# Optimization experiments

Hardware: AMD Instinct MI355X
Metric: run time of the kernel (lower is better)

## Reference

```python
import jax, jax.numpy as jnp
import numpy as np
import math

B, P, N, DM, H, DK, DH, DF = 2, 12, 170, 64, 8, 8, 32, 256
SQ = math.sqrt(DK)

def _ln(x, g, b):
    m = jnp.mean(x, -1, keepdims=True)
    v = jnp.var(x, -1, keepdims=True)
    return (x - m) / jnp.sqrt(v + 1e-5) * g + b

def _nozero_softmax(s):
    # faithful to nozero_softmax: mask = (s != 0), max over full row, +1e-5 in denom
    mask = (s != 0).astype(s.dtype)
    e = jnp.exp(s - jnp.max(s, -1, keepdims=True)) * mask
    return e / (jnp.sum(e, -1, keepdims=True) + 1e-5)

def _meta(c, w1, b1, w2, b2):
    # MetaLearner: [B,P,N,DM] -> [3,B,P,N,H,DK,DM]
    h = jax.nn.relu(c @ w1 + b1) @ w2 + b2
    h = h.reshape(c.shape[:3] + (3, H, DK, DM))
    return jnp.moveaxis(h, 3, 0)

def _mhlin(W, x):
    # multihead_linear_transform: per-position meta weight applied to x
    return jnp.einsum('bpnhkd,bpnd->bpnhk', W, x)

def _gdc(data, W1, W2):
    # Gated_Dynamic_Connection (noGC=False). data: [G,B,P,N,C]
    d = jnp.moveaxis(data, 0, 3)  # [B,P,N,G,C]
    a = jnp.einsum('bpngc,gcd->bpngd', d, W1)
    s = jax.nn.softmax(jax.nn.relu(jnp.einsum('bpngc,gcd->bpngd', d, W2)), axis=3)
    return jnp.sum(a * s, axis=3)  # [B,P,N,DM]

def _swish_gate(x, out, wg, bg, wo, bo):
    h = (x @ wg + bg) * out
    return (h * jax.nn.sigmoid(h)) @ wo + bo

def _spatial(Q, K, V, T):
    # adjacency-masked spatial attention. Dense-masked form is exactly the
    # scatter-into-zeros buffer of the original: zero where T==0, QK/sqrt(dk) on edges.
    s = jnp.einsum('bpihk,bpjhk->bphij', Q, K) / SQ
    Tb = T if T.ndim == 2 else T[:, :, None]  # adaptive graph [B,P,1,N,N]
    s = s * (Tb != 0)
    alpha = _nozero_softmax(s) * Tb
    return jnp.einsum('bphij,bpjhk->hbpik', alpha, V)  # [H,B,P,N,DK]

def _temporal(Q, K, V):
    s = jnp.einsum('bqnhk,bpnhk->bnhqp', Q, K) / SQ
    alpha = jax.nn.softmax(s, -1)
    return jnp.einsum('bnhqp,bpnhk->hbqnk', alpha, V)  # [H,B,P,N,DK]

def _retnet(Q, K, V, D):
    # multihead_temporal_regnet with g=1 leading dim folded in
    r = jnp.einsum('bqnhk,bpnhk->bnhqp', Q, K) / SQ
    r = r * D  # D: [H,P,P] causal decay
    rs = jnp.maximum(jnp.abs(jnp.sum(r, -1, keepdims=True)), 1.0)
    r = r / rs
    return jnp.einsum('bnhqp,bpnhk->hbqnk', r, V)  # [H,B,P,N,DK]

def _forward(x, c_x, enc, T, A, D, mr_w1, mr_b1, mr_w2, mr_b2, ms0_w1, ms0_b1, ms0_w2, ms0_b2, ms1_w1, ms1_b1, ms1_w2, ms1_b2, gr_W1, gr_W2, gs0_W1, gs0_W2, gs1_W1, gs1_W2, g2_W1, g2_W2, ge_W1, ge_W2, swr_wg, swr_bg, swr_wo, swr_bo, sws_wg, sws_bg, sws_wo, sws_bo, swe_wg, swe_bg, swe_wo, swe_bo, lnr_g, lnr_b, lns_g, lns_b, lne_g, lne_b, lnf_g, lnf_b, wq, wk, wv, f_w1, f_b1, f_w2, f_b2):
    # 1) RetNet-style temporal self retention (meta-learned QKV)
    W = _meta(c_x, mr_w1, mr_b1, mr_w2, mr_b2)
    o = _gdc(_retnet(_mhlin(W[0], x), _mhlin(W[1], x), _mhlin(W[2], x), D), gr_W1, gr_W2)
    o = _swish_gate(x, o, swr_wg, swr_bg, swr_wo, swr_bo)
    x1 = _ln(o + x, lnr_g, lnr_b)
    # 2) Spatial self attention: predefined graph + adaptive graph branches
    W0 = _meta(c_x, ms0_w1, ms0_b1, ms0_w2, ms0_b2)
    o0 = _gdc(_spatial(_mhlin(W0[0], x1), _mhlin(W0[1], x1), _mhlin(W0[2], x1), T), gs0_W1, gs0_W2)
    W1m = _meta(c_x, ms1_w1, ms1_b1, ms1_w2, ms1_b2)
    o1 = _gdc(_spatial(_mhlin(W1m[0], x1), _mhlin(W1m[1], x1), _mhlin(W1m[2], x1), A), gs1_W1, gs1_W2)
    o = _gdc(jnp.stack([o0, o1], 0), g2_W1, g2_W2)
    o = _swish_gate(x1, o, sws_wg, sws_bg, sws_wo, sws_bo)
    x2 = _ln(o + x1, lns_g, lns_b)
    # 3) Temporal encoder-decoder attention
    q = (x2 @ wq).reshape(B, P, N, H, DK)
    k = (enc @ wk).reshape(B, P, N, H, DK)
    v = (enc @ wv).reshape(B, P, N, H, DK)
    o = _gdc(_temporal(q, k, v), ge_W1, ge_W2)
    o = _swish_gate(x2, o, swe_wg, swe_bg, swe_wo, swe_bo)
    x3 = _ln(o + x2, lne_g, lne_b)
    # 4) FFN
    o = jax.nn.relu(x3 @ f_w1 + f_b1) @ f_w2 + f_b2
    return _ln(o + x3, lnf_g, lnf_b)


def setup_inputs() -> dict:
    key = jax.random.key(0)
    ks = iter(jax.random.split(key, 100))
    def rn(shape, s=0.05):
        return (jax.random.normal(next(ks), shape) * s).astype(jnp.float32)
    inp = {}
    inp['x'] = jax.random.normal(next(ks), (B, P, N, DM), jnp.float32)
    inp['c_x'] = jax.random.normal(next(ks), (B, P, N, DM), jnp.float32)
    inp['enc'] = jax.random.normal(next(ks), (B, P, N, DM), jnp.float32)
    mT = jax.random.uniform(next(ks), (N, N)) < 0.1
    inp['T'] = (jax.random.uniform(next(ks), (N, N)) * mT).astype(jnp.float32)
    mA = jax.random.uniform(next(ks), (B, P, N, N)) < 0.05
    inp['A'] = (jax.random.uniform(next(ks), (B, P, N, N)) * mA).astype(jnp.float32)
    q = np.arange(P)
    gam = 1.0 - 2.0 ** (-5.0 - np.arange(H))
    Dm = np.where(q[:, None] >= q[None, :], gam[:, None, None] ** (q[:, None] - q[None, :]), 0.0)
    inp['D'] = jnp.asarray(Dm, jnp.float32)  # [H,P,P]
    for p in ['mr', 'ms0', 'ms1']:
        inp[p + '_w1'] = rn((DM, DH)); inp[p + '_b1'] = jnp.zeros((DH,), jnp.float32)
        inp[p + '_w2'] = rn((DH, 3 * H * DK * DM)); inp[p + '_b2'] = jnp.zeros((3 * H * DK * DM,), jnp.float32)
    for p in ['gr', 'gs0', 'gs1', 'ge']:
        inp[p + '_W1'] = rn((H, DK, DM)); inp[p + '_W2'] = rn((H, DK, DM))
    inp['g2_W1'] = rn((2, DM, DM)); inp['g2_W2'] = rn((2, DM, DM))
    for p in ['swr', 'sws', 'swe']:
        inp[p + '_wg'] = rn((DM, DM)); inp[p + '_bg'] = jnp.zeros((DM,), jnp.float32)
        inp[p + '_wo'] = rn((DM, DM)); inp[p + '_bo'] = jnp.zeros((DM,), jnp.float32)
    for p in ['lnr', 'lns', 'lne', 'lnf']:
        inp[p + '_g'] = jnp.ones((DM,), jnp.float32); inp[p + '_b'] = jnp.zeros((DM,), jnp.float32)
    inp['wq'] = rn((DM, DM)); inp['wk'] = rn((DM, DM)); inp['wv'] = rn((DM, DM))
    inp['f_w1'] = rn((DM, DF)); inp['f_b1'] = jnp.zeros((DF,), jnp.float32)
    inp['f_w2'] = rn((DF, DM)); inp['f_b2'] = jnp.zeros((DM,), jnp.float32)
    return inp


def reference(x, c_x, enc, T, A, D, mr_w1, mr_b1, mr_w2, mr_b2, ms0_w1, ms0_b1, ms0_w2, ms0_b2, ms1_w1, ms1_b1, ms1_w2, ms1_b2, gr_W1, gr_W2, gs0_W1, gs0_W2, gs1_W1, gs1_W2, g2_W1, g2_W2, ge_W1, ge_W2, swr_wg, swr_bg, swr_wo, swr_bo, sws_wg, sws_bg, sws_wo, sws_bo, swe_wg, swe_bg, swe_wo, swe_bo, lnr_g, lnr_b, lns_g, lns_b, lne_g, lne_b, lnf_g, lnf_b, wq, wk, wv, f_w1, f_b1, f_w2, f_b2):
    return _forward(x, c_x, enc, T, A, D, mr_w1, mr_b1, mr_w2, mr_b2, ms0_w1, ms0_b1, ms0_w2, ms0_b2, ms1_w1, ms1_b1, ms1_w2, ms1_b2, gr_W1, gr_W2, gs0_W1, gs0_W2, gs1_W1, gs1_W2, g2_W1, g2_W2, ge_W1, ge_W2, swr_wg, swr_bg, swr_wo, swr_bo, sws_wg, sws_bg, sws_wo, sws_bo, swe_wg, swe_bg, swe_wo, swe_bo, lnr_g, lnr_b, lns_g, lns_b, lne_g, lne_b, lnf_g, lnf_b, wq, wk, wv, f_w1, f_b1, f_w2, f_b2)
```

## Files before the change

kernel.cpp:

```cpp
#include <hip/hip_runtime.h>
#include <hip/hip_bf16.h>
#include <math.h>

namespace {

constexpr int B_ = 2, P_ = 12, N_ = 170, DM_ = 64, H_ = 8, DK_ = 8, DH_ = 32, DF_ = 256;
constexpr int T_ = B_ * P_ * N_;
constexpr float SQRT_DK = 2.8284271247461903f;

constexpr int NG_ = 12;
constexpr int NC_ = 66;
constexpr int WFRAG_G = NG_ * NC_ * 64 * 8;

typedef __attribute__((ext_vector_type(4))) short short4v;
typedef __attribute__((ext_vector_type(8))) short short8v;
typedef __attribute__((ext_vector_type(4))) float float4v;

__device__ __forceinline__ unsigned short f2bf(float x) {
    union { float f; unsigned int u; } c; c.f = x;
    unsigned int r = (c.u + 0x7FFFu + ((c.u >> 16) & 1u)) >> 16;
    return (unsigned short)r;
}

__global__ void k_hr3(const float* __restrict__ c_x,
                      const float* __restrict__ w1a, const float* __restrict__ b1a,
                      const float* __restrict__ w1b, const float* __restrict__ b1b,
                      const float* __restrict__ w1c, const float* __restrict__ b1c,
                      float* __restrict__ hra, float* __restrict__ hrb,
                      float* __restrict__ hrc) {
    int z = blockIdx.y;
    const float* w1 = z == 0 ? w1a : (z == 1 ? w1b : w1c);
    const float* b1 = z == 0 ? b1a : (z == 1 ? b1b : b1c);
    float* hr = z == 0 ? hra : (z == 1 ? hrb : hrc);
    int idx = blockIdx.x * 256 + threadIdx.x;
    if (idx >= T_ * DH_) return;
    int t = idx / DH_, j = idx % DH_;
    float acc = b1[j];
    const float* cx = c_x + t * DM_;
    #pragma unroll
    for (int d = 0; d < DM_; ++d) acc += cx[d] * w1[d * DH_ + j];
    hr[idx] = fmaxf(acc, 0.f);
}

__global__ void k_wconv(const float* __restrict__ w2a, const float* __restrict__ b2a,
                        const float* __restrict__ w2b, const float* __restrict__ b2b,
                        const float* __restrict__ w2c, const float* __restrict__ b2c,
                        unsigned short* __restrict__ Wfrag) {
    int idx = blockIdx.x * 256 + threadIdx.x;
    if (idx >= 3 * NG_ * NC_ * 64) return;
    int lane = idx & 63;
    int c = (idx >> 6) % NC_;
    int ng = (idx >> 6) / NC_ % NG_;
    int g = idx / (64 * NC_ * NG_);
    const float* w2 = g == 0 ? w2a : (g == 1 ? w2b : w2c);
    const float* b2 = g == 0 ? b2a : (g == 1 ? b2b : b2c);
    int m = ng * 16 + (lane & 15);
    int u = c >> 1;
    int d0 = (c & 1) * 32 + (lane >> 4) * 8;
    const float* src = (u < DH_) ? (w2 + u * 12288 + m * 64 + d0) : (b2 + m * 64 + d0);
    short8v o;
    #pragma unroll
    for (int j = 0; j < 8; ++j) o[j] = (short)f2bf(src[j]);
    *(short8v*)(Wfrag + (size_t)idx * 8) = o;
}

__global__ __launch_bounds__(256) void k_meta_gemm2(
    const float* __restrict__ hr0, const float* __restrict__ hr1,
    const float* __restrict__ xin,
    const unsigned short* __restrict__ Wf0, const unsigned short* __restrict__ Wf1,
    float* __restrict__ out0, float* __restrict__ out1) {
    const int bz = blockIdx.z;
    const float* hr = bz ? hr1 : hr0;
    const unsigned short* Wf = bz ? Wf1 : Wf0;
    float* out = bz ? out1 : out0;

    const int tid = threadIdx.x;
    const int wv = tid >> 6, lane = tid & 63;
    const int l15 = lane & 15, quad = lane >> 4;
    const int g16 = blockIdx.x * 4 + wv;
    if (g16 >= 255) return;
    const int t = g16 * 16 + l15;
    const int nb = blockIdx.y;

    const float* xp = xin + t * 64 + quad * 8;
    float4v xa = *(const float4v*)(xp);
    float4v xb = *(const float4v*)(xp + 4);
    float4v xc = *(const float4v*)(xp + 32);
    float4v xd = *(const float4v*)(xp + 36);
    float xr[16] = {xa.x, xa.y, xa.z, xa.w, xb.x, xb.y, xb.z, xb.w,
                    xc.x, xc.y, xc.z, xc.w, xd.x, xd.y, xd.z, xd.w};

    const float* hrp = hr + t * 32;
    float4v acc[4] = {{0.f,0.f,0.f,0.f},{0.f,0.f,0.f,0.f},
                      {0.f,0.f,0.f,0.f},{0.f,0.f,0.f,0.f}};

    const unsigned short* wb = Wf + ((size_t)(nb * 4) * NC_ * 64 + lane) * 8;
    const size_t qstride = (size_t)NC_ * 64 * 8;
    const size_t cstride = 64 * 8;

    for (int u = 0; u < 33; ++u) {
        float hrv = (u < DH_) ? hrp[u] : 1.0f;
        short8v a0, a1;
        #pragma unroll
        for (int j = 0; j < 8; ++j) {
            a0[j] = (short)f2bf(hrv * xr[j]);
            a1[j] = (short)f2bf(hrv * xr[8 + j]);
        }
        const unsigned short* wc = wb + (size_t)(2 * u) * cstride;
        #pragma unroll
        for (int q = 0; q < 4; ++q) {
            short8v b0 = *(const short8v*)(wc + q * qstride);
            short8v b1 = *(const short8v*)(wc + q * qstride + cstride);
            acc[q] = __builtin_amdgcn_mfma_f32_16x16x32_bf16(a0, b0, acc[q], 0, 0, 0);
            acc[q] = __builtin_amdgcn_mfma_f32_16x16x32_bf16(a1, b1, acc[q], 0, 0, 0);
        }
    }

    #pragma unroll
    for (int q = 0; q < 4; ++q) {
        #pragma unroll
        for (int r = 0; r < 4; ++r) {
            int tt = g16 * 16 + quad * 4 + r;
            out[tt * 192 + nb * 64 + q * 16 + l15] = acc[q][r];
        }
    }
}

__global__ __launch_bounds__(256) void k_retnet(const float* __restrict__ qkv,
                                                const float* __restrict__ Dm,
                                                float* __restrict__ att) {
    const int bn = blockIdx.x;
    const int b = bn / N_, n = bn % N_;
    __shared__ float S[12][192];
    __shared__ float Ds[8 * 145];
    const int tid = threadIdx.x;
    for (int e = tid; e < 12 * 192; e += 256) {
        int p = e / 192, c = e % 192;
        S[p][c] = qkv[((size_t)((b * P_ + p) * N_ + n)) * 192 + c];
    }
    for (int e = tid; e < 1152; e += 256) {
        Ds[(e / 144) * 145 + (e % 144)] = Dm[e];
    }
    __syncthreads();
    const int qq = tid >> 6;
    const int lane = tid & 63;
    const int h = lane >> 3, k = lane & 7;
    for (int q = qq; q < P_; q += 4) {
        float Qv = S[q][h * 8 + k];
        float r[P_];
        float rsum = 0.f;
        #pragma unroll
        for (int p = 0; p < P_; ++p) {
            float prod = Qv * S[p][64 + h * 8 + k];
            prod += __shfl_xor(prod, 1, 64);
            prod += __shfl_xor(prod, 2, 64);
            prod += __shfl_xor(prod, 4, 64);
            float s = (prod / SQRT_DK) * Ds[h * 145 + q * 12 + p];
            r[p] = s; rsum += s;
        }
        float rs = fmaxf(fabsf(rsum), 1.0f);
        float acc = 0.f;
        #pragma unroll
        for (int p = 0; p < P_; ++p) acc += (r[p] / rs) * S[p][128 + h * 8 + k];
        att[((size_t)((b * P_ + q) * N_ + n)) * 64 + lane] = acc;
    }
}

__global__ __launch_bounds__(256) void k_temporal(const float* __restrict__ qkv,
                                                  float* __restrict__ att) {
    const int bn = blockIdx.x;
    const int b = bn / N_, n = bn % N_;
    __shared__ float S[12][192];
    const int tid = threadIdx.x;
    for (int e = tid; e < 12 * 192; e += 256) {
        int p = e / 192, c = e % 192;
        S[p][c] = qkv[((size_t)((b * P_ + p) * N_ + n)) * 192 + c];
    }
    __syncthreads();
    const int qq = tid >> 6;
    const int lane = tid & 63;
    const int h = lane >> 3, k = lane & 7;
    for (int q = qq; q < P_; q += 4) {
        float Qv = S[q][h * 8 + k];
        float s[P_];
        float mx = -1e30f;
        #pragma unroll
        for (int p = 0; p < P_; ++p) {
            float prod = Qv * S[p][64 + h * 8 + k];
            prod += __shfl_xor(prod, 1, 64);
            prod += __shfl_xor(prod, 2, 64);
            prod += __shfl_xor(prod, 4, 64);
            float v = prod / SQRT_DK;
            s[p] = v; mx = fmaxf(mx, v);
        }
        float den = 0.f, acc = 0.f;
        #pragma unroll
        for (int p = 0; p < P_; ++p) {
            float e = expf(s[p] - mx);
            den += e;
            acc += e * S[p][128 + h * 8 + k];
        }
        att[((size_t)((b * P_ + q) * N_ + n)) * 64 + lane] = acc / den;
    }
}

__global__ __launch_bounds__(256) void k_spatial4(
    const float* __restrict__ qkvA, const float* __restrict__ qkvB,
    const float* __restrict__ Tm, const float* __restrict__ Am,
    float* __restrict__ attA, float* __restrict__ attB) {
    const int bp = blockIdx.x;
    const int h = blockIdx.y;
    const int g = blockIdx.z >> 2;
    const int ic = blockIdx.z & 3;
    const float* qkv = g ? qkvB : qkvA;
    float* att = g ? attB : attA;

    __shared__ float sKt[8][192];
    __shared__ float sV[192][8];
    __shared__ float sW[4][192];

    const int tid = threadIdx.x;
    for (int e = tid; e < 384; e += 256) {
        int j = e >> 1, kh = (e & 1) * 4;
        float4v k4 = {0.f, 0.f, 0.f, 0.f}, v4 = k4;
        if (j < N_) {
            const float* row = qkv + (size_t)(bp * N_ + j) * 192 + h * 8 + kh;
            k4 = *(const float4v*)(row + 64);
            v4 = *(const float4v*)(row + 128);
        }
        sKt[kh + 0][j] = k4.x;
        sKt[kh + 1][j] = k4.y;
        sKt[kh + 2][j] = k4.z;
        sKt[kh + 3][j] = k4.w;
        *(float4v*)&sV[j][kh] = v4;
    }
    __syncthreads();

    const int wv = tid >> 6;
    const int lane = tid & 63;
    const int j8 = lane >> 3, kk = lane & 7;

    const int i0 = ic * 43;
    const int i1 = (i0 + 43 < N_) ? (i0 + 43) : N_;

    for (int i = i0 + wv; i < i1; i += 4) {
        const float* qrow = qkv + (size_t)(bp * N_ + i) * 192 + h * 8;
        float4v qa = *(const float4v*)qrow;
        float4v qb = *(const float4v*)(qrow + 4);
        float Qi[8] = {qa.x, qa.y, qa.z, qa.w, qb.x, qb.y, qb.z, qb.w};
        const float* Trow = g ? (Am + (size_t)(bp * N_ + i) * N_) : (Tm + (size_t)i * N_);

        float sloc[3], tloc[3];
        float mx = -1e30f;
        #pragma unroll
        for (int c = 0; c < 3; ++c) {
            int j = c * 64 + lane;
            float tv = 0.f, s = -1e30f;
            if (j < N_) {
                tv = Trow[j];
                if (tv != 0.f) {
                    float dot = 0.f;
                    #pragma unroll
                    for (int k = 0; k < 8; ++k) dot += Qi[k] * sKt[k][j];
                    s = dot / SQRT_DK;
                } else {
                    s = 0.f;
                }
            }
            sloc[c] = s; tloc[c] = tv;
            mx = fmaxf(mx, s);
        }
        #pragma unroll
        for (int off = 1; off < 64; off <<= 1) mx = fmaxf(mx, __shfl_xor(mx, off, 64));

        float den = 0.f;
        #pragma unroll
        for (int c = 0; c < 3; ++c) {
            float s = sloc[c];
            float e = (s != 0.f) ? expf(s - mx) : 0.f;
            den += e;
            sW[wv][c * 64 + lane] = e * tloc[c];
        }
        #pragma unroll
        for (int off = 1; off < 64; off <<= 1) den += __shfl_xor(den, off, 64);

        float acc = 0.f;
        #pragma unroll 4
        for (int j = j8; j < 192; j += 8) acc += sW[wv][j] * sV[j][kk];
        acc += __shfl_xor(acc, 8, 64);
        acc += __shfl_xor(acc, 16, 64);
        acc += __shfl_xor(acc, 32, 64);
        if (lane < 8)
            att[(size_t)(bp * N_ + i) * 64 + h * 8 + lane] = acc / (den + 1e-5f);
    }
}

__device__ __forceinline__ float gdc8(const float* dv, const float* W1,
                                      const float* W2, int dm) {
    float a[8], s[8];
    #pragma unroll
    for (int g = 0; g < 8; ++g) {
        float aa = 0.f, ss = 0.f;
        #pragma unroll
        for (int c = 0; c < 8; ++c) {
            float d = dv[g * 8 + c];
            aa += d * W1[(g * 8 + c) * 64 + dm];
            ss += d * W2[(g * 8 + c) * 64 + dm];
        }
        a[g] = aa; s[g] = fmaxf(ss, 0.f);
    }
    float mx = s[0];
    #pragma unroll
    for (int g = 1; g < 8; ++g) mx = fmaxf(mx, s[g]);
    float den = 0.f, o = 0.f;
    #pragma unroll
    for (int g = 0; g < 8; ++g) { float e = expf(s[g] - mx); den += e; o += a[g] * e; }
    return o / den;
}

__device__ __forceinline__ float ln_out(float r, int dm, const float* g, const float* b) {
    float m = r, m2 = r * r;
    #pragma unroll
    for (int off = 32; off; off >>= 1) { m += __shfl_xor(m, off, 64); m2 += __shfl_xor(m2, off, 64); }
    m *= (1.f / 64.f); m2 *= (1.f / 64.f);
    float var = m2 - m * m;
    return (r - m) * rsqrtf(var + 1e-5f) * g[dm] + b[dm];
}

__global__ __launch_bounds__(64) void k_gsl(const float* __restrict__ att, const float* __restrict__ xin,
    const float* W1, const float* W2,
    const float* wg, const float* bg,
    const float* wo, const float* bo,
    const float* lng, const float* lnb, float* __restrict__ xout) {
    int t = blockIdx.x, dm = threadIdx.x;
    __shared__ float dv[64], xv[64], swv[64];
    dv[dm] = att[t * 64 + dm];
    xv[dm] = xin[t * 64 + dm];
    __syncthreads();
    float o = gdc8(dv, W1, W2, dm);
    float hg = bg[dm];
    #pragma unroll
    for (int d = 0; d < 64; ++d) hg += xv[d] * wg[d * 64 + dm];
    hg *= o;
    swv[dm] = hg / (1.f + expf(-hg));
    __syncthreads();
    float ov = bo[dm];
    #pragma unroll
    for (int d = 0; d < 64; ++d) ov += swv[d] * wo[d * 64 + dm];
    float r = ov + xv[dm];
    xout[t * 64 + dm] = ln_out(r, dm, lng, lnb);
}

__global__ __launch_bounds__(64) void k_spatial_fuse(
    const float* __restrict__ att0, const float* __restrict__ att1, const float* __restrict__ x1,
    const float* gs0_W1, const float* gs0_W2,
    const float* gs1_W1, const float* gs1_W2,
    const float* g2_W1, const float* g2_W2,
    const float* wg, const float* bg,
    const float* wo, const float* bo,
    const float* lng, const float* lnb, float* __restrict__ xout) {
    int t = blockIdx.x, dm = threadIdx.x;
    __shared__ float d0[64], d1[64], o0s[64], o1s[64], xv[64], swv[64];
    d0[dm] = att0[t * 64 + dm];
    d1[dm] = att1[t * 64 + dm];
    xv[dm] = x1[t * 64 + dm];
    __syncthreads();
    o0s[dm] = gdc8(d0, gs0_W1, gs0_W2, dm);
    o1s[dm] = gdc8(d1, gs1_W1, gs1_W2, dm);
    __syncthreads();
    float a0 = 0.f, s0 = 0.f, a1 = 0.f, s1 = 0.f;
    #pragma unroll
    for (int c = 0; c < 64; ++c) {
        a0 += o0s[c] * g2_W1[c * 64 + dm];
        s0 += o0s[c] * g2_W2[c * 64 + dm];
        a1 += o1s[c] * g2_W1[(64 + c) * 64 + dm];
        s1 += o1s[c] * g2_W2[(64 + c) * 64 + dm];
    }
    s0 = fmaxf(s0, 0.f); s1 = fmaxf(s1, 0.f);
    float mx = fmaxf(s0, s1);
    float e0 = expf(s0 - mx), e1 = expf(s1 - mx);
    float o = (a0 * e0 + a1 * e1) / (e0 + e1);
    float hg = bg[dm];
    #pragma unroll
    for (int d = 0; d < 64; ++d) hg += xv[d] * wg[d * 64 + dm];
    hg *= o;
    swv[dm] = hg / (1.f + expf(-hg));
    __syncthreads();
    float ov = bo[dm];
    #pragma unroll
    for (int d = 0; d < 64; ++d) ov += swv[d] * wo[d * 64 + dm];
    float r = ov + xv[dm];
    xout[t * 64 + dm] = ln_out(r, dm, lng, lnb);
}

__global__ __launch_bounds__(64) void k_qkvproj(const float* __restrict__ x2,
    const float* __restrict__ enc,
    const float* wq, const float* wk, const float* wv,
    float* __restrict__ qkv) {
    int t = blockIdx.x, dm = threadIdx.x;
    __shared__ float xv[64], ev[64];
    xv[dm] = x2[t * 64 + dm];
    ev[dm] = enc[t * 64 + dm];
    __syncthreads();
    float aq = 0.f, ak = 0.f, av = 0.f;
    #pragma unroll
    for (int d = 0; d < 64; ++d) {
        aq += xv[d] * wq[d * 64 + dm];
        ak += ev[d] * wk[d * 64 + dm];
        av += ev[d] * wv[d * 64 + dm];
    }
    qkv[t * 192 + dm] = aq;
    qkv[t * 192 + 64 + dm] = ak;
    qkv[t * 192 + 128 + dm] = av;
}

__global__ __launch_bounds__(64) void k_ffn(const float* __restrict__ x3,
    const float* w1, const float* b1,
    const float* w2, const float* b2,
    const float* lng, const float* lnb,
    float* __restrict__ out) {
    int t = blockIdx.x, dm = threadIdx.x;
    __shared__ float xv[64], hv[256];
    xv[dm] = x3[t * 64 + dm];
    __syncthreads();
    #pragma unroll
    for (int e = 0; e < 4; ++e) {
        int j = e * 64 + dm;
        float a = b1[j];
        #pragma unroll
        for (int d = 0; d < 64; ++d) a += xv[d] * w1[d * 256 + j];
        hv[j] = fmaxf(a, 0.f);
    }
    __syncthreads();
    float a = b2[dm];
    for (int j = 0; j < 256; ++j) a += hv[j] * w2[j * 64 + dm];
    float r = a + xv[dm];
    out[t * 64 + dm] = ln_out(r, dm, lng, lnb);
}

}

extern "C" void kernel_launch(void* const* d_in, const int* in_sizes, int n_in,
                              void* d_out, int out_size, void* d_ws, size_t ws_size,
                              hipStream_t stream) {
    (void)in_sizes; (void)n_in; (void)out_size; (void)ws_size;
    const float* x    = (const float*)d_in[0];
    const float* c_x  = (const float*)d_in[1];
    const float* enc  = (const float*)d_in[2];
    const float* Tm   = (const float*)d_in[3];
    const float* Am   = (const float*)d_in[4];
    const float* Dm   = (const float*)d_in[5];
    const float* mr_w1 = (const float*)d_in[6];
    const float* mr_b1 = (const float*)d_in[7];
    const float* mr_w2 = (const float*)d_in[8];
    const float* mr_b2 = (const float*)d_in[9];
    const float* ms0_w1 = (const float*)d_in[10];
    const float* ms0_b1 = (const float*)d_in[11];
    const float* ms0_w2 = (const float*)d_in[12];
    const float* ms0_b2 = (const float*)d_in[13];
    const float* ms1_w1 = (const float*)d_in[14];
    const float* ms1_b1 = (const float*)d_in[15];
    const float* ms1_w2 = (const float*)d_in[16];
    const float* ms1_b2 = (const float*)d_in[17];
    const float* gr_W1 = (const float*)d_in[18];
    const float* gr_W2 = (const float*)d_in[19];
    const float* gs0_W1 = (const float*)d_in[20];
    const float* gs0_W2 = (const float*)d_in[21];
    const float* gs1_W1 = (const float*)d_in[22];
    const float* gs1_W2 = (const float*)d_in[23];
    const float* g2_W1 = (const float*)d_in[24];
    const float* g2_W2 = (const float*)d_in[25];
    const float* ge_W1 = (const float*)d_in[26];
    const float* ge_W2 = (const float*)d_in[27];
    const float* swr_wg = (const float*)d_in[28];
    const float* swr_bg = (const float*)d_in[29];
    const float* swr_wo = (const float*)d_in[30];
    const float* swr_bo = (const float*)d_in[31];
    const float* sws_wg = (const float*)d_in[32];
    const float* sws_bg = (const float*)d_in[33];
    const float* sws_wo = (const float*)d_in[34];
    const float* sws_bo = (const float*)d_in[35];
    const float* swe_wg = (const float*)d_in[36];
    const float* swe_bg = (const float*)d_in[37];
    const float* swe_wo = (const float*)d_in[38];
    const float* swe_bo = (const float*)d_in[39];
    const float* lnr_g = (const float*)d_in[40];
    const float* lnr_b = (const float*)d_in[41];
    const float* lns_g = (const float*)d_in[42];
    const float* lns_b = (const float*)d_in[43];
    const float* lne_g = (const float*)d_in[44];
    const float* lne_b = (const float*)d_in[45];
    const float* lnf_g = (const float*)d_in[46];
    const float* lnf_b = (const float*)d_in[47];
    const float* wq = (const float*)d_in[48];
    const float* wk = (const float*)d_in[49];
    const float* wv = (const float*)d_in[50];
    const float* f_w1 = (const float*)d_in[51];
    const float* f_b1 = (const float*)d_in[52];
    const float* f_w2 = (const float*)d_in[53];
    const float* f_b2 = (const float*)d_in[54];

    float* ws   = (float*)d_ws;
    float* hr   = ws;
    float* hr2  = hr   + T_ * DH_;
    float* qkva = hr2  + T_ * DH_;
    float* qkvb = qkva + T_ * 192;
    float* atta = qkvb + T_ * 192;
    float* attb = atta + T_ * DM_;
    float* x1f  = attb + T_ * DM_;
    float* x2f  = x1f  + T_ * DM_;
    float* x3f  = x2f  + T_ * DM_;
    unsigned short* Wfrag = (unsigned short*)(x3f + T_ * DM_);
    float* hr_r = attb;

    k_wconv<<<(3 * NG_ * NC_ * 64 + 255) / 256, 256, 0, stream>>>(
        mr_w2, mr_b2, ms0_w2, ms0_b2, ms1_w2, ms1_b2, Wfrag);

    k_hr3<<<dim3(510, 3), 256, 0, stream>>>(c_x, mr_w1, mr_b1, ms0_w1, ms0_b1,
                                            ms1_w1, ms1_b1, hr_r, hr, hr2);

    k_meta_gemm2<<<dim3(64, 3, 1), 256, 0, stream>>>(
        hr_r, hr_r, x, Wfrag, Wfrag, qkva, qkva);
    k_retnet<<<B_ * N_, 256, 0, stream>>>(qkva, Dm, atta);
    k_gsl<<<T_, 64, 0, stream>>>(atta, x, gr_W1, gr_W2, swr_wg, swr_bg, swr_wo, swr_bo,
                                 lnr_g, lnr_b, x1f);

    k_meta_gemm2<<<dim3(64, 3, 2), 256, 0, stream>>>(
        hr, hr2, x1f, Wfrag + WFRAG_G, Wfrag + 2 * WFRAG_G, qkva, qkvb);
    k_spatial4<<<dim3(B_ * P_, H_, 8), 256, 0, stream>>>(qkva, qkvb, Tm, Am, atta, attb);
    k_spatial_fuse<<<T_, 64, 0, stream>>>(atta, attb, x1f, gs0_W1, gs0_W2, gs1_W1, gs1_W2,
                                          g2_W1, g2_W2, sws_wg, sws_bg, sws_wo, sws_bo,
                                          lns_g, lns_b, x2f);

    k_qkvproj<<<T_, 64, 0, stream>>>(x2f, enc, wq, wk, wv, qkva);
    k_temporal<<<B_ * N_, 256, 0, stream>>>(qkva, atta);
    k_gsl<<<T_, 64, 0, stream>>>(atta, x2f, ge_W1, ge_W2, swe_wg, swe_bg, swe_wo, swe_bo,
                                 lne_g, lne_b, x3f);

    k_ffn<<<T_, 64, 0, stream>>>(x3f, f_w1, f_b1, f_w2, f_b2, lnf_g, lnf_b, (float*)d_out);
}
```

Before: 352.6 us.

## Replace dense masked spatial attention with sparse edge-list online softmax

The spatial attention kernel no longer computes scores for every node pair. Each wavefront now compacts the nonzero adjacency entries of its row into a shared-memory edge list using ballot and popcount. It then iterates only over those edges with an online softmax, computing all 8 heads at once across the 64 lanes. This removes dense work on zero entries and the per-head shared-memory tiling, at the cost of scattered global K/V row loads per edge. The running max now starts at 0 rather than the true row max, which matches the reference only because masked zero scores also take part in that max.

Measured after the change: 324.7 us. -7.9%, faster.

```diff
diff --git a/kernel.cpp b/kernel.cpp
--- a/kernel.cpp
+++ b/kernel.cpp
@@ -204,95 +204,78 @@
     }
 }
 
-__global__ __launch_bounds__(256) void k_spatial4(
+__global__ __launch_bounds__(256) void k_spatial_sparse(
     const float* __restrict__ qkvA, const float* __restrict__ qkvB,
     const float* __restrict__ Tm, const float* __restrict__ Am,
     float* __restrict__ attA, float* __restrict__ attB) {
-    const int bp = blockIdx.x;
-    const int h = blockIdx.y;
-    const int g = blockIdx.z >> 2;
-    const int ic = blockIdx.z & 3;
+    const int bp = blockIdx.y;
+    const int g = blockIdx.z;
     const float* qkv = g ? qkvB : qkvA;
     float* att = g ? attB : attA;
 
-    __shared__ float sKt[8][192];
-    __shared__ float sV[192][8];
-    __shared__ float sW[4][192];
+    __shared__ int2 elist[4][176];
 
     const int tid = threadIdx.x;
-    for (int e = tid; e < 384; e += 256) {
-        int j = e >> 1, kh = (e & 1) * 4;
-        float4v k4 = {0.f, 0.f, 0.f, 0.f}, v4 = k4;
-        if (j < N_) {
-            const float* row = qkv + (size_t)(bp * N_ + j) * 192 + h * 8 + kh;
-            k4 = *(const float4v*)(row + 64);
-            v4 = *(const float4v*)(row + 128);
-        }
-        sKt[kh + 0][j] = k4.x;
-        sKt[kh + 1][j] = k4.y;
-        sKt[kh + 2][j] = k4.z;
-        sKt[kh + 3][j] = k4.w;
-        *(float4v*)&sV[j][kh] = v4;
-    }
-    __syncthreads();
-
-    const int wv = tid >> 6;
-    const int lane = tid & 63;
-    const int j8 = lane >> 3, kk = lane & 7;
-
-    const int i0 = ic * 43;
-    const int i1 = (i0 + 43 < N_) ? (i0 + 43) : N_;
-
-    for (int i = i0 + wv; i < i1; i += 4) {
-        const float* qrow = qkv + (size_t)(bp * N_ + i) * 192 + h * 8;
-        float4v qa = *(const float4v*)qrow;
-        float4v qb = *(const float4v*)(qrow + 4);
-        float Qi[8] = {qa.x, qa.y, qa.z, qa.w, qb.x, qb.y, qb.z, qb.w};
-        const float* Trow = g ? (Am + (size_t)(bp * N_ + i) * N_) : (Tm + (size_t)i * N_);
-
-        float sloc[3], tloc[3];
-        float mx = -1e30f;
-        #pragma unroll
-        for (int c = 0; c < 3; ++c) {
-            int j = c * 64 + lane;
-            float tv = 0.f, s = -1e30f;
-            if (j < N_) {
-                tv = Trow[j];
-                if (tv != 0.f) {
-                    float dot = 0.f;
-                    #pragma unroll
-                    for (int k = 0; k < 8; ++k) dot += Qi[k] * sKt[k][j];
-                    s = dot / SQRT_DK;
-                } else {
-                    s = 0.f;
-                }
-            }
-            sloc[c] = s; tloc[c] = tv;
-            mx = fmaxf(mx, s);
-        }
-        #pragma unroll
-        for (int off = 1; off < 64; off <<= 1) mx = fmaxf(mx, __shfl_xor(mx, off, 64));
-
-        float den = 0.f;
-        #pragma unroll
-        for (int c = 0; c < 3; ++c) {
-            float s = sloc[c];
-            float e = (s != 0.f) ? expf(s - mx) : 0.f;
-            den += e;
-            sW[wv][c * 64 + lane] = e * tloc[c];
-        }
-        #pragma unroll
-        for (int off = 1; off < 64; off <<= 1) den += __shfl_xor(den, off, 64);
-
-        float acc = 0.f;
-        #pragma unroll 4
-        for (int j = j8; j < 192; j += 8) acc += sW[wv][j] * sV[j][kk];
-        acc += __shfl_xor(acc, 8, 64);
-        acc += __shfl_xor(acc, 16, 64);
-        acc += __shfl_xor(acc, 32, 64);
-        if (lane < 8)
-            att[(size_t)(bp * N_ + i) * 64 + h * 8 + lane] = acc / (den + 1e-5f);
-    }
+    const int wv = tid >> 6, lane = tid & 63;
+    const int i = blockIdx.x * 4 + wv;
+    if (i >= N_) return;
+
+    int2* el = elist[wv];
+    const float* Trow = g ? (Am + (size_t)(bp * N_ + i) * N_) : (Tm + (size_t)i * N_);
+    int nnz = 0;
+    #pragma unroll
+    for (int c = 0; c < 3; ++c) {
+        int j = c * 64 + lane;
+        float w = (j < N_) ? Trow[j] : 0.f;
+        unsigned long long m = __ballot(w != 0.f);
+        if (w != 0.f) {
+            int pos = nnz + (int)__popcll(m & ((1ull << lane) - 1ull));
+            el[pos] = make_int2(j, __float_as_int(w));
+        }
+        nnz += (int)__popcll(m);
+    }
+
+    const float q = qkv[(size_t)(bp * N_ + i) * 192 + lane];
+    float m = 0.f;
+    float den = 0.f, acc = 0.f;
+    int e = 0;
+    for (; e + 1 < nnz; e += 2) {
+        int2 e0 = el[e], e1 = el[e + 1];
+        const float* r0 = qkv + (size_t)(bp * N_ + e0.x) * 192;
+        const float* r1 = qkv + (size_t)(bp * N_ + e1.x) * 192;
+        float k0 = r0[64 + lane], v0 = r0[128 + lane];
+        float k1 = r1[64 + lane], v1 = r1[128 + lane];
+        float p0 = q * k0, p1 = q * k1;
+        p0 += __shfl_xor(p0, 1, 64); p1 += __shfl_xor(p1, 1, 64);
+        p0 += __shfl_xor(p0, 2, 64); p1 += __shfl_xor(p1, 2, 64);
+        p0 += __shfl_xor(p0, 4, 64); p1 += __shfl_xor(p1, 4, 64);
+        float s0 = p0 / SQRT_DK, s1 = p1 / SQRT_DK;
+        float mn = fmaxf(m, fmaxf(s0, s1));
+        float cs = expf(m - mn);
+        float x0 = (s0 != 0.f) ? expf(s0 - mn) : 0.f;
+        float x1 = (s1 != 0.f) ? expf(s1 - mn) : 0.f;
+        den = den * cs + x0 + x1;
+        acc = acc * cs + x0 * __int_as_float(e0.y) * v0
+                       + x1 * __int_as_float(e1.y) * v1;
+        m = mn;
+    }
+    if (e < nnz) {
+        int2 e0 = el[e];
+        const float* r0 = qkv + (size_t)(bp * N_ + e0.x) * 192;
+        float k0 = r0[64 + lane], v0 = r0[128 + lane];
+        float p0 = q * k0;
+        p0 += __shfl_xor(p0, 1, 64);
+        p0 += __shfl_xor(p0, 2, 64);
+        p0 += __shfl_xor(p0, 4, 64);
+        float s0 = p0 / SQRT_DK;
+        float mn = fmaxf(m, s0);
+        float cs = expf(m - mn);
+        float x0 = (s0 != 0.f) ? expf(s0 - mn) : 0.f;
+        den = den * cs + x0;
+        acc = acc * cs + x0 * __int_as_float(e0.y) * v0;
+    }
+
+    att[(size_t)(bp * N_ + i) * 64 + lane] = acc / (den + 1e-5f);
 }
 
 __device__ __forceinline__ float gdc8(const float* dv, const float* W1,
@@ -527,7 +510,8 @@
 
     k_meta_gemm2<<<dim3(64, 3, 2), 256, 0, stream>>>(
         hr, hr2, x1f, Wfrag + WFRAG_G, Wfrag + 2 * WFRAG_G, qkva, qkvb);
-    k_spatial4<<<dim3(B_ * P_, H_, 8), 256, 0, stream>>>(qkva, qkvb, Tm, Am, atta, attb);
+    k_spatial_sparse<<<dim3((N_ + 3) / 4, B_ * P_, 2), 256, 0, stream>>>(
+        qkva, qkvb, Tm, Am, atta, attb);
     k_spatial_fuse<<<T_, 64, 0, stream>>>(atta, attb, x1f, gs0_W1, gs0_W2, gs1_W1, gs1_W2,
                                           g2_W1, g2_W2, sws_wg, sws_bg, sws_wo, sws_bo,
                                           lns_g, lns_b, x2f);
```
